# Optimization experiments

Hardware: AMD Instinct MI355X
Metric: run time of the kernel (lower is better)

## Reference

```python
import jax, jax.numpy as jnp
import numpy as np

HIDDEN = 2048
HEAD = 256
VDIM = 512  # double_v_dim=True -> 2*head_size
GAMMA = 0.96875
SCALE_BASE = 512.0  # xpos default


def _rotate_every_two(x):
    # (x0, x1, x2, x3, ...) -> (-x1, x0, -x3, x2, ...)
    x1 = x[..., ::2]
    x2 = x[..., 1::2]
    return jnp.stack((-x2, x1), axis=-1).reshape(x.shape)


def _xpos(x, downscale=False, offset=0):
    # Standard XPOS (rotary + exponential scaling) as used in RetNet repos.
    S, d = x.shape[1], x.shape[2]
    d2 = d // 2
    scale_vec = (jnp.arange(0, d, 2, dtype=jnp.float32) + 0.4 * d) / (1.4 * d)  # [d2]
    pos = jnp.arange(S + offset, dtype=jnp.float32)
    scale = scale_vec[None, :] ** (pos[:, None] / SCALE_BASE)  # [S+off, d2]
    inv_freq = 1.0 / (10000.0 ** (jnp.arange(d2, dtype=jnp.float32) / d2))
    sinusoid = pos[:, None] * inv_freq[None, :]  # [S+off, d2]
    sin, cos = jnp.sin(sinusoid), jnp.cos(sinusoid)
    scale, sin, cos = scale[-S:], sin[-S:], cos[-S:]
    if downscale:
        scale = 1.0 / scale
    sin_s = jnp.repeat(sin * scale, 2, axis=-1)  # duplicate_interleave -> [S, d]
    cos_s = jnp.repeat(cos * scale, 2, axis=-1)
    return x * cos_s[None] + _rotate_every_two(x) * sin_s[None]


def _decay_matrix(S):
    # D[n, m] = gamma^(n-m) for n >= m else 0 (NaN/overflow-safe)
    n = jnp.arange(S, dtype=jnp.float32)
    diff = n[:, None] - n[None, :]
    mask = diff >= 0
    return jnp.where(mask, GAMMA ** jnp.where(mask, diff, 0.0), 0.0)


def setup_inputs() -> dict:
    key = jax.random.key(0)
    k1, k2, k3, k4 = jax.random.split(key, 4)
    B, S = 4, 4096
    X = jax.random.normal(k1, (B, S, HIDDEN), dtype=jnp.float32)
    W_Q = jax.random.normal(k2, (HIDDEN, HEAD), dtype=jnp.float32) / HIDDEN
    W_K = jax.random.normal(k3, (HIDDEN, HEAD), dtype=jnp.float32) / HIDDEN
    W_V = jax.random.normal(k4, (HIDDEN, VDIM), dtype=jnp.float32) / HIDDEN
    return {"X": X, "W_Q": W_Q, "W_K": W_K, "W_V": W_V}


def reference(X, W_Q, W_K, W_V):
    S = X.shape[1]
    Q = _xpos(X @ W_Q)                      # [B, S, HEAD]
    K = _xpos(X @ W_K, downscale=True)      # [B, S, HEAD]
    V = X @ W_V                             # [B, S, VDIM]
    D = _decay_matrix(S)                    # [S, S]
    retention = jnp.einsum('bqd,bkd->bqk', Q, K) * D[None]  # [B, S, S]
    return retention @ V                    # [B, S, VDIM]
```

## Files before the change

kernel.cpp:

```cpp
#include <hip/hip_runtime.h>
#include <math.h>

#define NB 4
#define SEQ 4096
#define HID 2048
#define DH 256
#define DV 512
#define CHUNK 128
#define NCH 32
#define MROWS (NB * SEQ)
#define GAMMA 0.96875f
#define GAMMA_INV 1.0322580645161290f
#define LOG2_GAMMA (-0.045803689613124794f)
#define LOG2_10000 13.287712379549449f

typedef __attribute__((ext_vector_type(8))) short short8;
typedef __attribute__((ext_vector_type(4))) float floatx4;

__device__ __forceinline__ unsigned short bf16_rne(float v) {
    unsigned int u = __float_as_uint(v);
    u += 0x7fff + ((u >> 16) & 1);
    return (unsigned short)(u >> 16);
}
__device__ __forceinline__ float b2f(unsigned short h) {
    return __uint_as_float((unsigned int)h << 16);
}

__device__ __forceinline__ void gld16(const void* g, void* l) {
    __builtin_amdgcn_global_load_lds(
        reinterpret_cast<const __attribute__((address_space(1))) unsigned int*>(
            reinterpret_cast<uintptr_t>(g)),
        reinterpret_cast<__attribute__((address_space(3))) unsigned int*>(
            reinterpret_cast<uintptr_t>(l)),
        16, 0, 0);
}

__global__ __launch_bounds__(256) void xcvt_kernel(
    const float* __restrict__ X, unsigned short* __restrict__ Xb)
{
    const int i = blockIdx.x * 256 + threadIdx.x;
    float4 x = ((const float4*)X)[i];
    ushort4 h;
    h.x = bf16_rne(x.x); h.y = bf16_rne(x.y);
    h.z = bf16_rne(x.z); h.w = bf16_rne(x.w);
    ((ushort4*)Xb)[i] = h;
}

__global__ __launch_bounds__(256) void wcvt_kernel(
    const float* __restrict__ WQ, const float* __restrict__ WK,
    const float* __restrict__ WV, unsigned short* __restrict__ Bt)
{
    __shared__ unsigned short sh[64][65];
    const int bid = blockIdx.x;
    const int kt = bid & 31;
    const int ntile = bid >> 5;
    const int k0 = kt * 64, n0 = ntile * 64;

    const float* W; int ld, nl0;
    if (n0 < 256)      { W = WQ; ld = DH; nl0 = n0; }
    else if (n0 < 512) { W = WK; ld = DH; nl0 = n0 - 256; }
    else               { W = WV; ld = DV; nl0 = n0 - 512; }

    const int t = threadIdx.x;
#pragma unroll
    for (int p = 0; p < 4; p++) {
        const int kl = (t >> 4) + p * 16;
        const int ng = (t & 15) * 4;
        float4 w = *(const float4*)&W[(size_t)(k0 + kl) * ld + nl0 + ng];
        sh[kl][ng + 0] = bf16_rne(w.x);
        sh[kl][ng + 1] = bf16_rne(w.y);
        sh[kl][ng + 2] = bf16_rne(w.z);
        sh[kl][ng + 3] = bf16_rne(w.w);
    }
    __syncthreads();
#pragma unroll
    for (int p = 0; p < 4; p++) {
        const int nl = (t >> 4) + p * 16;
        const int kg = (t & 15) * 4;
        ushort4 h;
        h.x = sh[kg + 0][nl]; h.y = sh[kg + 1][nl];
        h.z = sh[kg + 2][nl]; h.w = sh[kg + 3][nl];
        *(ushort4*)&Bt[(size_t)(n0 + nl) * HID + k0 + kg] = h;
    }
}

__global__ __launch_bounds__(512, 2) void qkv_mfma_kernel(
    const unsigned short* __restrict__ Xb, const unsigned short* __restrict__ Bt,
    unsigned short* __restrict__ Qb, unsigned short* __restrict__ Kb,
    unsigned short* __restrict__ Kt, unsigned short* __restrict__ Vt)
{
    __shared__ unsigned short lds[2 * 32768];

    const int bid = blockIdx.x;
    const int xcd = bid & 7;
    const int idx = bid >> 3;
    const int mt  = (xcd << 3) | (idx >> 2);
    const int nt  = idx & 3;
    const int m0 = mt * 256, n0 = nt * 256;

    const int t = threadIdx.x;
    const int w = t >> 6, lane = t & 63;
    const int wr = w >> 2;
    const int wc = w & 3;

    floatx4 acc[8][4];
#pragma unroll
    for (int i = 0; i < 8; i++)
#pragma unroll
        for (int j = 0; j < 4; j++) acc[i][j] = (floatx4)0.0f;

    const int rl = lane >> 3;
    const int sg = (lane & 7) ^ rl;

    const int fr = lane & 15, g = lane >> 4;
    const int x7 = fr & 7;
    const int soff0 = ((g ^ x7) << 3);
    const int soff1 = (((4 | g) ^ x7) << 3);

#define STAGE_HT(isB, h, dbuf, kt)                                            \
    {                                                                         \
        const unsigned short* gsrc =                                          \
            ((isB) ? Bt + (size_t)(n0 + (h) * 128 + w * 16 + rl) * HID        \
                   : Xb + (size_t)(m0 + (h) * 128 + w * 16 + rl) * HID)       \
            + (size_t)(kt) * 64 + sg * 8;                                     \
        unsigned short* ldst = &lds[(dbuf) * 32768 + ((isB) ? 16384 : 0)      \
                                    + ((h) * 128 + w * 16) * 64];             \
        gld16(gsrc, ldst);                                                    \
        gld16(gsrc + (size_t)8 * HID, ldst + 8 * 64);                         \
    }

#define READ_A(ih)                                                            \
    _Pragma("unroll")                                                         \
    for (int i2 = 0; i2 < 4; i2++) {                                          \
        const int row = wr * 128 + ((ih) * 4 + i2) * 16 + fr;                 \
        ah[i2][0] = *(const short8*)&lds[cb + row * 64 + soff0];              \
        ah[i2][1] = *(const short8*)&lds[cb + row * 64 + soff1];              \
    }

#define READ_B(jh)                                                            \
    _Pragma("unroll")                                                         \
    for (int j2 = 0; j2 < 2; j2++) {                                          \
        const int row = wc * 64 + ((jh) * 2 + j2) * 16 + fr;                  \
        bh[(jh) * 2 + j2][0] = *(const short8*)&lds[cb + 16384 + row * 64 + soff0]; \
        bh[(jh) * 2 + j2][1] = *(const short8*)&lds[cb + 16384 + row * 64 + soff1]; \
    }

#define MFMA16(ib, jb)                                                        \
    _Pragma("unroll")                                                         \
    for (int i2 = 0; i2 < 4; i2++)                                            \
        _Pragma("unroll")                                                     \
        for (int j2 = 0; j2 < 2; j2++) {                                      \
            acc[(ib) + i2][(jb) + j2] = __builtin_amdgcn_mfma_f32_16x16x32_bf16( \
                ah[i2][0], bh[(jb) + j2][0], acc[(ib) + i2][(jb) + j2], 0, 0, 0); \
            acc[(ib) + i2][(jb) + j2] = __builtin_amdgcn_mfma_f32_16x16x32_bf16( \
                ah[i2][1], bh[(jb) + j2][1], acc[(ib) + i2][(jb) + j2], 0, 0, 0); \
        }

    STAGE_HT(0, 0, 0, 0); STAGE_HT(0, 1, 0, 0);
    STAGE_HT(1, 0, 0, 0); STAGE_HT(1, 1, 0, 0);
    asm volatile("s_waitcnt vmcnt(0)" ::: "memory");
    __builtin_amdgcn_s_barrier();
    __builtin_amdgcn_sched_barrier(0);

    int cur = 0;
    for (int kt = 0; kt < 32; ++kt) {
        const int nxt = cur ^ 1;
        if (kt + 1 < 32) {
            STAGE_HT(0, 0, nxt, kt + 1); STAGE_HT(0, 1, nxt, kt + 1);
            STAGE_HT(1, 0, nxt, kt + 1); STAGE_HT(1, 1, nxt, kt + 1);
        }
        const int cb = cur * 32768;
        short8 ah[4][2], bh[4][2];

        READ_A(0); READ_B(0);
        __builtin_amdgcn_s_barrier();
        __builtin_amdgcn_sched_barrier(0);
        __builtin_amdgcn_s_setprio(1);
        MFMA16(0, 0);
        __builtin_amdgcn_s_setprio(0);
        __builtin_amdgcn_s_barrier();
        __builtin_amdgcn_sched_barrier(0);

        READ_B(1);
        __builtin_amdgcn_s_barrier();
        __builtin_amdgcn_sched_barrier(0);
        __builtin_amdgcn_s_setprio(1);
        MFMA16(0, 2);
        __builtin_amdgcn_s_setprio(0);
        __builtin_amdgcn_s_barrier();
        __builtin_amdgcn_sched_barrier(0);

        READ_A(1);
        __builtin_amdgcn_s_barrier();
        __builtin_amdgcn_sched_barrier(0);
        __builtin_amdgcn_s_setprio(1);
        MFMA16(4, 0);
        __builtin_amdgcn_s_setprio(0);
        __builtin_amdgcn_s_barrier();
        __builtin_amdgcn_sched_barrier(0);

        __builtin_amdgcn_s_setprio(1);
        MFMA16(4, 2);
        __builtin_amdgcn_s_setprio(0);
        asm volatile("s_waitcnt vmcnt(0)" ::: "memory");
        __builtin_amdgcn_s_barrier();
        __builtin_amdgcn_sched_barrier(0);
        cur = nxt;
    }
#undef STAGE_HT
#undef READ_A
#undef READ_B
#undef MFMA16

    const int cl = lane & 15, rq = (lane >> 4) << 2;
    if (n0 >= 512) {
#pragma unroll
        for (int i = 0; i < 8; i++)
#pragma unroll
            for (int j = 0; j < 4; j++) {
                const int c = n0 - 512 + wc * 64 + j * 16 + cl;
#pragma unroll
                for (int r = 0; r < 4; r++) {
                    const int m = m0 + wr * 128 + i * 16 + rq + r;
                    Vt[(size_t)c * MROWS + m] = bf16_rne(acc[i][j][r]);
                }
            }
    } else {
        const bool isQ = (n0 < 256);
        unsigned short* dst = isQ ? Qb : Kb;
        const float sgn = isQ ? 1.f : -1.f;
#pragma unroll
        for (int j = 0; j < 4; j++) {
            const int c = wc * 64 + j * 16 + cl;
            const float jj = (float)(c >> 1);
            const float sv = (2.f * jj + 0.4f * 256.f) * (1.f / (1.4f * 256.f));
            const float l2sv = __log2f(sv) * sgn * (1.f / 512.f);
            const float invf = exp2f(jj * (-LOG2_10000 / 128.f));
            const bool odd = (c & 1) != 0;
#pragma unroll
            for (int i = 0; i < 8; i++) {
#pragma unroll
                for (int r = 0; r < 4; r++) {
                    const int m = m0 + wr * 128 + i * 16 + rq + r;
                    const float s = (float)(m & (SEQ - 1));
                    const float x = acc[i][j][r];
                    const float p = __shfl_xor(x, 1, 64);
                    const float sc = exp2f(s * l2sv);
                    const float ang = s * invf;
                    const float sn = __sinf(ang), cs = __cosf(ang);
                    const float o = odd ? sc * (x * cs + p * sn)
                                        : sc * (x * cs - p * sn);
                    const unsigned short hv = bf16_rne(o);
                    dst[(size_t)m * DH + c] = hv;
                    if (!isQ) Kt[(size_t)c * MROWS + m] = hv;
                }
            }
        }
    }
}

__global__ __launch_bounds__(512, 1) void chunk_kv_kernel(
    const unsigned short* __restrict__ Kt, const unsigned short* __restrict__ Vt,
    float* __restrict__ Ut)
{
    __shared__ unsigned short As[128 * 32];
    __shared__ unsigned short Bs[128 * 32];

    const int bid = blockIdx.x;
    const int dht = bid & 1;
    const int vq  = (bid >> 1) & 3;
    const int c   = (bid >> 3) & 31;
    const int b   = bid >> 8;
    const int dh0 = dht * 128, dv0 = vq * 128;
    const int row0 = b * SEQ + c * CHUNK;

    const int t = threadIdx.x;
    const int w = t >> 6, lane = t & 63;
    const int wm = (w & 1) << 6;
    const int wn = (w >> 1) << 5;
    const int srow = lane >> 2, scol = (lane & 3) * 8;
    const int fr = lane & 15, fq = (lane >> 4) * 8;

    floatx4 acc[4][2];
#pragma unroll
    for (int i = 0; i < 4; i++)
#pragma unroll
        for (int j = 0; j < 2; j++) acc[i][j] = (floatx4)0.0f;

    const int kr = t >> 2, kc = (t & 3) * 8;

    for (int i0 = 0; i0 < CHUNK; i0 += 32) {
        __syncthreads();
        gld16(&Vt[(size_t)(dv0 + w * 16 + srow) * MROWS + row0 + i0 + scol],
              &As[(w * 16) * 32]);
        {
            const unsigned short* src = &Kt[(size_t)(dh0 + kr) * MROWS + row0 + i0 + kc];
            ushort4 k0v = *(const ushort4*)src;
            ushort4 k1v = *(const ushort4*)(src + 4);
            float g = exp2f((float)(CHUNK - i0 - kc) * LOG2_GAMMA);
            ushort4 h0, h1;
            h0.x = bf16_rne(b2f(k0v.x) * g); g *= GAMMA_INV;
            h0.y = bf16_rne(b2f(k0v.y) * g); g *= GAMMA_INV;
            h0.z = bf16_rne(b2f(k0v.z) * g); g *= GAMMA_INV;
            h0.w = bf16_rne(b2f(k0v.w) * g); g *= GAMMA_INV;
            h1.x = bf16_rne(b2f(k1v.x) * g); g *= GAMMA_INV;
            h1.y = bf16_rne(b2f(k1v.y) * g); g *= GAMMA_INV;
            h1.z = bf16_rne(b2f(k1v.z) * g); g *= GAMMA_INV;
            h1.w = bf16_rne(b2f(k1v.w) * g);
            *(ushort4*)&Bs[kr * 32 + kc] = h0;
            *(ushort4*)&Bs[kr * 32 + kc + 4] = h1;
        }
        __syncthreads();
        short8 a[4], bb[2];
#pragma unroll
        for (int i = 0; i < 4; i++)
            a[i] = *(const short8*)&As[(wm + i * 16 + fr) * 32 + fq];
#pragma unroll
        for (int j = 0; j < 2; j++)
            bb[j] = *(const short8*)&Bs[(wn + j * 16 + fr) * 32 + fq];
#pragma unroll
        for (int i = 0; i < 4; i++)
#pragma unroll
            for (int j = 0; j < 2; j++)
                acc[i][j] = __builtin_amdgcn_mfma_f32_16x16x32_bf16(a[i], bb[j], acc[i][j], 0, 0, 0);
    }

    const int cl = lane & 15, rq = (lane >> 4) << 2;
    const size_t ubase = ((size_t)(b * NCH + c) * DV + dv0) * DH + dh0;
#pragma unroll
    for (int i = 0; i < 4; i++)
#pragma unroll
        for (int j = 0; j < 2; j++) {
            const int n = wn + j * 16 + cl;
#pragma unroll
            for (int r = 0; r < 4; r++) {
                const int m = wm + i * 16 + rq + r;
                Ut[ubase + (size_t)m * DH + n] = acc[i][j][r];
            }
        }
}

__global__ __launch_bounds__(256) void scan_kernel(
    const float* __restrict__ Ut, unsigned short* __restrict__ Sb)
{
    const int t = blockIdx.x * 256 + threadIdx.x;
    const int b = t >> 17;
    const int r = t & 131071;
    const float gC = exp2f((float)CHUNK * LOG2_GAMMA);
    float s = 0.f;
    const size_t base = (size_t)b * NCH * 131072 + r;
    for (int c = 0; c < NCH; c++) {
        const size_t off = base + (size_t)c * 131072;
        const float u = Ut[off];
        Sb[off] = bf16_rne(s);
        s = gC * s + u;
    }
}

__global__ __launch_bounds__(512, 1) void out_mfma_kernel(
    const unsigned short* __restrict__ Qb, const unsigned short* __restrict__ Kb,
    const unsigned short* __restrict__ Vt, const unsigned short* __restrict__ Sb,
    float* __restrict__ out)
{
    __shared__ unsigned short Pa[128 * 136];
    __shared__ unsigned short As[2 * 128 * 32];
    __shared__ unsigned short Bs[2 * 128 * 32];

    const int bid = blockIdx.x;
    const int vq = bid & 3;
    const int c  = (bid >> 2) & 31;
    const int b  = bid >> 7;
    const int dv0 = vq * 128;
    const int row0 = b * SEQ + c * CHUNK;

    const int t = threadIdx.x;
    const int w = t >> 6, lane = t & 63;
    const int wm = (w & 1) << 6;
    const int wn = (w >> 1) << 5;
    const int fr = lane & 15, fq = (lane >> 4) * 8;
    const int cl = lane & 15, rq = (lane >> 4) << 2;
    const int srow = lane >> 2, scol = (lane & 3) * 8;

    floatx4 acc[4][2];
#pragma unroll
    for (int i = 0; i < 4; i++)
#pragma unroll
        for (int j = 0; j < 2; j++) acc[i][j] = (floatx4)0.0f;

    for (int d0 = 0; d0 < DH; d0 += 64) {
        __syncthreads();
        gld16(&Qb[(size_t)(row0 + w * 16 + srow) * DH + d0 + scol], &As[(w * 16) * 32]);
        gld16(&Qb[(size_t)(row0 + w * 16 + srow) * DH + d0 + 32 + scol], &As[4096 + (w * 16) * 32]);
        gld16(&Kb[(size_t)(row0 + w * 16 + srow) * DH + d0 + scol], &Bs[(w * 16) * 32]);
        gld16(&Kb[(size_t)(row0 + w * 16 + srow) * DH + d0 + 32 + scol], &Bs[4096 + (w * 16) * 32]);
        __syncthreads();
#pragma nounroll
        for (int s = 0; s < 2; s++) {
            short8 a[4], bb[2];
#pragma unroll
            for (int i = 0; i < 4; i++)
                a[i] = *(const short8*)&As[s * 4096 + (wm + i * 16 + fr) * 32 + fq];
#pragma unroll
            for (int j = 0; j < 2; j++)
                bb[j] = *(const short8*)&Bs[s * 4096 + (wn + j * 16 + fr) * 32 + fq];
#pragma unroll
            for (int i = 0; i < 4; i++)
#pragma unroll
                for (int j = 0; j < 2; j++)
                    acc[i][j] = __builtin_amdgcn_mfma_f32_16x16x32_bf16(a[i], bb[j], acc[i][j], 0, 0, 0);
        }
    }

#pragma unroll
    for (int i = 0; i < 4; i++)
#pragma unroll
        for (int j = 0; j < 2; j++) {
            const int jj = wn + j * 16 + cl;
#pragma unroll
            for (int r = 0; r < 4; r++) {
                const int ii = wm + i * 16 + rq + r;
                const int diff = ii - jj;
                const float v = (diff >= 0) ? acc[i][j][r] * exp2f((float)diff * LOG2_GAMMA) : 0.f;
                Pa[ii * 136 + jj] = bf16_rne(v);
            }
            acc[i][j] = (floatx4)0.0f;
        }

    for (int k0 = 0; k0 < CHUNK; k0 += 64) {
        __syncthreads();
        gld16(&Vt[(size_t)(dv0 + w * 16 + srow) * MROWS + row0 + k0 + scol], &Bs[(w * 16) * 32]);
        gld16(&Vt[(size_t)(dv0 + w * 16 + srow) * MROWS + row0 + k0 + 32 + scol], &Bs[4096 + (w * 16) * 32]);
        __syncthreads();
#pragma nounroll
        for (int s = 0; s < 2; s++) {
            short8 a[4], bb[2];
#pragma unroll
            for (int i = 0; i < 4; i++)
                a[i] = *(const short8*)&Pa[(wm + i * 16 + fr) * 136 + k0 + s * 32 + fq];
#pragma unroll
            for (int j = 0; j < 2; j++)
                bb[j] = *(const short8*)&Bs[s * 4096 + (wn + j * 16 + fr) * 32 + fq];
#pragma unroll
            for (int i = 0; i < 4; i++)
#pragma unroll
                for (int j = 0; j < 2; j++)
                    acc[i][j] = __builtin_amdgcn_mfma_f32_16x16x32_bf16(a[i], bb[j], acc[i][j], 0, 0, 0);
        }
    }

    const size_t sbbase = ((size_t)(b * NCH + c) * DV + dv0) * DH;
    const int xr = t >> 2, xc = (t & 3) * 8;
    const float gx = exp2f((float)xr * LOG2_GAMMA);
    for (int d0 = 0; d0 < DH; d0 += 64) {
        __syncthreads();
#pragma unroll
        for (int s = 0; s < 2; s++) {
            const unsigned short* src = &Qb[(size_t)(row0 + xr) * DH + d0 + s * 32 + xc];
            ushort4 q0 = *(const ushort4*)src;
            ushort4 q1 = *(const ushort4*)(src + 4);
            ushort4 h0, h1;
            h0.x = bf16_rne(b2f(q0.x) * gx); h0.y = bf16_rne(b2f(q0.y) * gx);
            h0.z = bf16_rne(b2f(q0.z) * gx); h0.w = bf16_rne(b2f(q0.w) * gx);
            h1.x = bf16_rne(b2f(q1.x) * gx); h1.y = bf16_rne(b2f(q1.y) * gx);
            h1.z = bf16_rne(b2f(q1.z) * gx); h1.w = bf16_rne(b2f(q1.w) * gx);
            *(ushort4*)&As[s * 4096 + xr * 32 + xc] = h0;
            *(ushort4*)&As[s * 4096 + xr * 32 + xc + 4] = h1;
        }
        gld16(&Sb[sbbase + (size_t)(w * 16 + srow) * DH + d0 + scol], &Bs[(w * 16) * 32]);
        gld16(&Sb[sbbase + (size_t)(w * 16 + srow) * DH + d0 + 32 + scol], &Bs[4096 + (w * 16) * 32]);
        __syncthreads();
#pragma nounroll
        for (int s = 0; s < 2; s++) {
            short8 a[4], bb[2];
#pragma unroll
            for (int i = 0; i < 4; i++)
                a[i] = *(const short8*)&As[s * 4096 + (wm + i * 16 + fr) * 32 + fq];
#pragma unroll
            for (int j = 0; j < 2; j++)
                bb[j] = *(const short8*)&Bs[s * 4096 + (wn + j * 16 + fr) * 32 + fq];
#pragma unroll
            for (int i = 0; i < 4; i++)
#pragma unroll
                for (int j = 0; j < 2; j++)
                    acc[i][j] = __builtin_amdgcn_mfma_f32_16x16x32_bf16(a[i], bb[j], acc[i][j], 0, 0, 0);
        }
    }

#pragma unroll
    for (int i = 0; i < 4; i++)
#pragma unroll
        for (int j = 0; j < 2; j++) {
            const int dv = dv0 + wn + j * 16 + cl;
#pragma unroll
            for (int r = 0; r < 4; r++) {
                const int m = row0 + wm + i * 16 + rq + r;
                out[(size_t)m * DV + dv] = acc[i][j][r];
            }
        }
}

extern "C" void kernel_launch(void* const* d_in, const int* in_sizes, int n_in,
                              void* d_out, int out_size, void* d_ws, size_t ws_size,
                              hipStream_t stream) {
    const float* X  = (const float*)d_in[0];
    const float* WQ = (const float*)d_in[1];
    const float* WK = (const float*)d_in[2];
    const float* WV = (const float*)d_in[3];
    float* out = (float*)d_out;

    char* ws = (char*)d_ws;
    unsigned short* Qb = (unsigned short*)ws;
    unsigned short* Kb = Qb + (size_t)MROWS * DH;
    unsigned short* Kt = Kb + (size_t)MROWS * DH;
    unsigned short* Vt = Kt + (size_t)MROWS * DH;
    unsigned short* Sb = Vt + (size_t)MROWS * DV;
    float*          Ut = (float*)(Sb + (size_t)NB * NCH * DV * DH);
    unsigned short* Xb = (unsigned short*)Ut;
    unsigned short* Bt = (unsigned short*)(Ut + (size_t)NB * NCH * DV * DH);

    xcvt_kernel<<<(MROWS * HID / 4) / 256, 256, 0, stream>>>(X, Xb);
    wcvt_kernel<<<512, 256, 0, stream>>>(WQ, WK, WV, Bt);
    qkv_mfma_kernel<<<256, 512, 0, stream>>>(Xb, Bt, Qb, Kb, Kt, Vt);
    chunk_kv_kernel<<<1024, 512, 0, stream>>>(Kt, Vt, Ut);
    scan_kernel<<<2048, 256, 0, stream>>>(Ut, Sb);
    out_mfma_kernel<<<512, 512, 0, stream>>>(Qb, Kb, Vt, Sb, out);
}
```

Baseline: 367.7 us.

## Use XOR-swizzled LDS tiles and single-shot chunk loads in chunk_kv and out kernels

The chunk_kv kernel now stages the whole 128-wide chunk of V and decay-scaled K into LDS at once, with XOR-swizzled 16-byte slots. This replaces four sync-separated 32-wide steps, and launch bounds are relaxed to allow two blocks per CU. The out kernel switches its Q/K, V and state tiles from split 32-column halves to 64-column rows with an XOR swizzle, meant to cut LDS bank conflicts on the MFMA fragment reads. The cost is larger LDS use in chunk_kv and more index arithmetic, and the bigger LDS footprint may limit the occupancy that the new launch bound is aiming for.

```diff
diff --git a/kernel.cpp b/kernel.cpp
--- a/kernel.cpp
+++ b/kernel.cpp
@@ -259,12 +259,12 @@
     }
 }
 
-__global__ __launch_bounds__(512, 1) void chunk_kv_kernel(
+__global__ __launch_bounds__(512, 2) void chunk_kv_kernel(
     const unsigned short* __restrict__ Kt, const unsigned short* __restrict__ Vt,
     float* __restrict__ Ut)
 {
-    __shared__ unsigned short As[128 * 32];
-    __shared__ unsigned short Bs[128 * 32];
+    __shared__ unsigned short As[128 * 128];
+    __shared__ unsigned short Bs[128 * 128];
 
     const int bid = blockIdx.x;
     const int dht = bid & 1;
@@ -278,8 +278,7 @@
     const int w = t >> 6, lane = t & 63;
     const int wm = (w & 1) << 6;
     const int wn = (w >> 1) << 5;
-    const int srow = lane >> 2, scol = (lane & 3) * 8;
-    const int fr = lane & 15, fq = (lane >> 4) * 8;
+    const int fr = lane & 15, g = lane >> 4;
 
     floatx4 acc[4][2];
 #pragma unroll
@@ -287,37 +286,52 @@
 #pragma unroll
         for (int j = 0; j < 2; j++) acc[i][j] = (floatx4)0.0f;
 
-    const int kr = t >> 2, kc = (t & 3) * 8;
-
-    for (int i0 = 0; i0 < CHUNK; i0 += 32) {
-        __syncthreads();
-        gld16(&Vt[(size_t)(dv0 + w * 16 + srow) * MROWS + row0 + i0 + scol],
-              &As[(w * 16) * 32]);
-        {
-            const unsigned short* src = &Kt[(size_t)(dh0 + kr) * MROWS + row0 + i0 + kc];
+    {
+        const int ar = lane >> 4, asl = lane & 15;
+#pragma unroll
+        for (int q = 0; q < 4; q++) {
+            const int row = w * 16 + q * 4 + ar;
+            const int ssl = asl ^ (row & 15);
+            gld16(&Vt[(size_t)(dv0 + row) * MROWS + row0 + ssl * 8],
+                  &As[(w * 16 + q * 4) * 128]);
+        }
+    }
+    {
+        const int kr = t >> 2, kc4 = t & 3;
+#pragma unroll
+        for (int p = 0; p < 4; p++) {
+            const int col = kc4 * 8 + p * 32;
+            const unsigned short* src = &Kt[(size_t)(dh0 + kr) * MROWS + row0 + col];
             ushort4 k0v = *(const ushort4*)src;
             ushort4 k1v = *(const ushort4*)(src + 4);
-            float g = exp2f((float)(CHUNK - i0 - kc) * LOG2_GAMMA);
+            float gsc = exp2f((float)(CHUNK - col) * LOG2_GAMMA);
             ushort4 h0, h1;
-            h0.x = bf16_rne(b2f(k0v.x) * g); g *= GAMMA_INV;
-            h0.y = bf16_rne(b2f(k0v.y) * g); g *= GAMMA_INV;
-            h0.z = bf16_rne(b2f(k0v.z) * g); g *= GAMMA_INV;
-            h0.w = bf16_rne(b2f(k0v.w) * g); g *= GAMMA_INV;
-            h1.x = bf16_rne(b2f(k1v.x) * g); g *= GAMMA_INV;
-            h1.y = bf16_rne(b2f(k1v.y) * g); g *= GAMMA_INV;
-            h1.z = bf16_rne(b2f(k1v.z) * g); g *= GAMMA_INV;
-            h1.w = bf16_rne(b2f(k1v.w) * g);
-            *(ushort4*)&Bs[kr * 32 + kc] = h0;
-            *(ushort4*)&Bs[kr * 32 + kc + 4] = h1;
-        }
-        __syncthreads();
+            h0.x = bf16_rne(b2f(k0v.x) * gsc); gsc *= GAMMA_INV;
+            h0.y = bf16_rne(b2f(k0v.y) * gsc); gsc *= GAMMA_INV;
+            h0.z = bf16_rne(b2f(k0v.z) * gsc); gsc *= GAMMA_INV;
+            h0.w = bf16_rne(b2f(k0v.w) * gsc); gsc *= GAMMA_INV;
+            h1.x = bf16_rne(b2f(k1v.x) * gsc); gsc *= GAMMA_INV;
+            h1.y = bf16_rne(b2f(k1v.y) * gsc); gsc *= GAMMA_INV;
+            h1.z = bf16_rne(b2f(k1v.z) * gsc); gsc *= GAMMA_INV;
+            h1.w = bf16_rne(b2f(k1v.w) * gsc);
+            const int wsl = (kc4 + p * 4) ^ (kr & 15);
+            *(ushort4*)&Bs[kr * 128 + wsl * 8] = h0;
+            *(ushort4*)&Bs[kr * 128 + wsl * 8 + 4] = h1;
+        }
+    }
+    __syncthreads();
+
+#pragma nounroll
+    for (int s = 0; s < 4; s++) {
         short8 a[4], bb[2];
 #pragma unroll
         for (int i = 0; i < 4; i++)
-            a[i] = *(const short8*)&As[(wm + i * 16 + fr) * 32 + fq];
+            a[i] = *(const short8*)&As[(wm + i * 16 + fr) * 128
+                                       + (((s * 4 + g) ^ fr) << 3)];
 #pragma unroll
         for (int j = 0; j < 2; j++)
-            bb[j] = *(const short8*)&Bs[(wn + j * 16 + fr) * 32 + fq];
+            bb[j] = *(const short8*)&Bs[(wn + j * 16 + fr) * 128
+                                        + (((s * 4 + g) ^ fr) << 3)];
 #pragma unroll
         for (int i = 0; i < 4; i++)
 #pragma unroll
@@ -363,8 +377,8 @@
     float* __restrict__ out)
 {
     __shared__ unsigned short Pa[128 * 136];
-    __shared__ unsigned short As[2 * 128 * 32];
-    __shared__ unsigned short Bs[2 * 128 * 32];
+    __shared__ unsigned short As[128 * 64];
+    __shared__ unsigned short Bs[128 * 64];
 
     const int bid = blockIdx.x;
     const int vq = bid & 3;
@@ -377,9 +391,11 @@
     const int w = t >> 6, lane = t & 63;
     const int wm = (w & 1) << 6;
     const int wn = (w >> 1) << 5;
-    const int fr = lane & 15, fq = (lane >> 4) * 8;
+    const int fr = lane & 15, g = lane >> 4, fq = g * 8;
     const int cl = lane & 15, rq = (lane >> 4) << 2;
-    const int srow = lane >> 2, scol = (lane & 3) * 8;
+    const int rl8 = lane >> 3, sl8 = lane & 7;
+    const int ssl8 = sl8 ^ rl8;
+    const int x7 = fr & 7;
 
     floatx4 acc[4][2];
 #pragma unroll
@@ -389,20 +405,26 @@
 
     for (int d0 = 0; d0 < DH; d0 += 64) {
         __syncthreads();
-        gld16(&Qb[(size_t)(row0 + w * 16 + srow) * DH + d0 + scol], &As[(w * 16) * 32]);
-        gld16(&Qb[(size_t)(row0 + w * 16 + srow) * DH + d0 + 32 + scol], &As[4096 + (w * 16) * 32]);
-        gld16(&Kb[(size_t)(row0 + w * 16 + srow) * DH + d0 + scol], &Bs[(w * 16) * 32]);
-        gld16(&Kb[(size_t)(row0 + w * 16 + srow) * DH + d0 + 32 + scol], &Bs[4096 + (w * 16) * 32]);
+#pragma unroll
+        for (int q = 0; q < 2; q++) {
+            const int row = w * 16 + q * 8 + rl8;
+            gld16(&Qb[(size_t)(row0 + row) * DH + d0 + ssl8 * 8],
+                  &As[(w * 16 + q * 8) * 64]);
+            gld16(&Kb[(size_t)(row0 + row) * DH + d0 + ssl8 * 8],
+                  &Bs[(w * 16 + q * 8) * 64]);
+        }
         __syncthreads();
 #pragma nounroll
         for (int s = 0; s < 2; s++) {
             short8 a[4], bb[2];
 #pragma unroll
             for (int i = 0; i < 4; i++)
-                a[i] = *(const short8*)&As[s * 4096 + (wm + i * 16 + fr) * 32 + fq];
+                a[i] = *(const short8*)&As[(wm + i * 16 + fr) * 64
+                                           + (((s * 4 + g) ^ x7) << 3)];
 #pragma unroll
             for (int j = 0; j < 2; j++)
-                bb[j] = *(const short8*)&Bs[s * 4096 + (wn + j * 16 + fr) * 32 + fq];
+                bb[j] = *(const short8*)&Bs[(wn + j * 16 + fr) * 64
+                                            + (((s * 4 + g) ^ x7) << 3)];
 #pragma unroll
             for (int i = 0; i < 4; i++)
 #pragma unroll
@@ -428,8 +450,12 @@
 
     for (int k0 = 0; k0 < CHUNK; k0 += 64) {
         __syncthreads();
-        gld16(&Vt[(size_t)(dv0 + w * 16 + srow) * MROWS + row0 + k0 + scol], &Bs[(w * 16) * 32]);
-        gld16(&Vt[(size_t)(dv0 + w * 16 + srow) * MROWS + row0 + k0 + 32 + scol], &Bs[4096 + (w * 16) * 32]);
+#pragma unroll
+        for (int q = 0; q < 2; q++) {
+            const int row = w * 16 + q * 8 + rl8;
+            gld16(&Vt[(size_t)(dv0 + row) * MROWS + row0 + k0 + ssl8 * 8],
+                  &Bs[(w * 16 + q * 8) * 64]);
+        }
         __syncthreads();
 #pragma nounroll
         for (int s = 0; s < 2; s++) {
@@ -439,7 +465,8 @@
                 a[i] = *(const short8*)&Pa[(wm + i * 16 + fr) * 136 + k0 + s * 32 + fq];
 #pragma unroll
             for (int j = 0; j < 2; j++)
-                bb[j] = *(const short8*)&Bs[s * 4096 + (wn + j * 16 + fr) * 32 + fq];
+                bb[j] = *(const short8*)&Bs[(wn + j * 16 + fr) * 64
+                                            + (((s * 4 + g) ^ x7) << 3)];
 #pragma unroll
             for (int i = 0; i < 4; i++)
 #pragma unroll
@@ -449,13 +476,14 @@
     }
 
     const size_t sbbase = ((size_t)(b * NCH + c) * DV + dv0) * DH;
-    const int xr = t >> 2, xc = (t & 3) * 8;
+    const int xr = t >> 2, xc4 = t & 3;
     const float gx = exp2f((float)xr * LOG2_GAMMA);
     for (int d0 = 0; d0 < DH; d0 += 64) {
         __syncthreads();
 #pragma unroll
         for (int s = 0; s < 2; s++) {
-            const unsigned short* src = &Qb[(size_t)(row0 + xr) * DH + d0 + s * 32 + xc];
+            const int col = s * 32 + xc4 * 8;
+            const unsigned short* src = &Qb[(size_t)(row0 + xr) * DH + d0 + col];
             ushort4 q0 = *(const ushort4*)src;
             ushort4 q1 = *(const ushort4*)(src + 4);
             ushort4 h0, h1;
@@ -463,21 +491,28 @@
             h0.z = bf16_rne(b2f(q0.z) * gx); h0.w = bf16_rne(b2f(q0.w) * gx);
             h1.x = bf16_rne(b2f(q1.x) * gx); h1.y = bf16_rne(b2f(q1.y) * gx);
             h1.z = bf16_rne(b2f(q1.z) * gx); h1.w = bf16_rne(b2f(q1.w) * gx);
-            *(ushort4*)&As[s * 4096 + xr * 32 + xc] = h0;
-            *(ushort4*)&As[s * 4096 + xr * 32 + xc + 4] = h1;
-        }
-        gld16(&Sb[sbbase + (size_t)(w * 16 + srow) * DH + d0 + scol], &Bs[(w * 16) * 32]);
-        gld16(&Sb[sbbase + (size_t)(w * 16 + srow) * DH + d0 + 32 + scol], &Bs[4096 + (w * 16) * 32]);
+            const int wsl = (s * 4 + xc4) ^ (xr & 7);
+            *(ushort4*)&As[xr * 64 + wsl * 8] = h0;
+            *(ushort4*)&As[xr * 64 + wsl * 8 + 4] = h1;
+        }
+#pragma unroll
+        for (int q = 0; q < 2; q++) {
+            const int row = w * 16 + q * 8 + rl8;
+            gld16(&Sb[sbbase + (size_t)row * DH + d0 + ssl8 * 8],
+                  &Bs[(w * 16 + q * 8) * 64]);
+        }
         __syncthreads();
 #pragma nounroll
         for (int s = 0; s < 2; s++) {
             short8 a[4], bb[2];
 #pragma unroll
             for (int i = 0; i < 4; i++)
-                a[i] = *(const short8*)&As[s * 4096 + (wm + i * 16 + fr) * 32 + fq];
+                a[i] = *(const short8*)&As[(wm + i * 16 + fr) * 64
+                                           + (((s * 4 + g) ^ x7) << 3)];
 #pragma unroll
             for (int j = 0; j < 2; j++)
-                bb[j] = *(const short8*)&Bs[s * 4096 + (wn + j * 16 + fr) * 32 + fq];
+                bb[j] = *(const short8*)&Bs[(wn + j * 16 + fr) * 64
+                                            + (((s * 4 + g) ^ x7) << 3)];
 #pragma unroll
             for (int i = 0; i < 4; i++)
 #pragma unroll
```

Result: no change. 363.6 us (-1.1%).
